# Kernel tuning notes

Hardware: AMD Instinct MI355X
Metric: run time of the kernel (lower is better)

The kernel has to match this reference:

```python
import jax, jax.numpy as jnp
import numpy as np
import math

B, S, IN, H, M = 4, 2048, 256, 128, 128  # mem_dim must equal hidden_size


def _xavier(key, shape):
    fan_in, fan_out = shape[0], shape[-1]
    lim = math.sqrt(6.0 / (fan_in + fan_out))
    return jax.random.uniform(key, shape, jnp.float32, -lim, lim)


def setup_inputs() -> dict:
    key = jax.random.key(0)
    ks = jax.random.split(key, 8)
    return dict(
        x=jax.random.normal(ks[0], (B, S, IN), jnp.float32),
        c0=jnp.zeros((M, M), jnp.float32),   # init_hidden matrix memory
        n0=jnp.zeros((M, 1), jnp.float32),   # init_hidden normalizer
        w_q=_xavier(ks[1], (IN, H)), b_q=jnp.zeros((H,), jnp.float32),
        w_k=_xavier(ks[2], (IN, M)), b_k=jnp.zeros((M,), jnp.float32),
        w_v=_xavier(ks[3], (IN, M)), b_v=jnp.zeros((M,), jnp.float32),
        w_i=_xavier(ks[4], (IN, 1)), b_i=jnp.zeros((1,), jnp.float32),
        w_f=_xavier(ks[5], (IN, 1)), b_f=jnp.zeros((1,), jnp.float32),
        w_o=_xavier(ks[6], (IN, H)), b_o=jnp.zeros((H,), jnp.float32),
    )


def reference(x, c0, n0, w_q, b_q, w_k, b_k, w_v, b_v, w_i, b_i, w_f, b_f, w_o, b_o):
    Bb, Ss, Ii = x.shape
    Mm = w_k.shape[1]
    Hh = w_q.shape[1]
    xf = x.reshape(Bb * Ss, Ii)                                  # [N, IN]
    q = xf @ w_q + b_q                                           # [N, H]
    k = (xf @ w_k + b_k) * (1.0 / math.sqrt(Mm))                 # [N, M]
    v = xf @ w_v + b_v                                           # [N, M]
    i_t = jnp.exp(xf @ w_i + b_i)                                # [N, 1]
    f_t = jax.nn.sigmoid(xf @ w_f + b_f)                         # [N, 1]
    # Original loop never updates c_prev: c_t[n] = f[n]*c0 + i[n]*outer(v[n], k[n])
    c = f_t[:, :, None] * c0[None] + i_t[:, :, None] * (v[:, :, None] * k[:, None, :])  # [N, M, M]
    n = f_t[:, :, None] * n0[None] + i_t[:, :, None] * k[:, :, None]                    # [N, M, 1]
    c = c.reshape(Bb, Ss, Mm, Mm)
    n = n.reshape(Bb, Ss, Mm, 1)
    q4 = q.reshape(Bb, Ss, Hh)
    nq = jnp.einsum('bsm,bsm->bs', n[..., 0], q4)                # n^T q
    denom = jnp.maximum(jnp.abs(nq), 1.0)[..., None]             # max(|n^T q|, 1)
    h_tilde = jnp.einsum('bsmk,bsk->bsm', c, q4) / denom         # (c_t q) / denom
    o = jax.nn.sigmoid(xf @ w_o + b_o).reshape(Bb, Ss, Hh)
    h = o * h_tilde                                              # [B, S, H]
    return (h, c, n)
```

## Files before the change

kernel.cpp:

```cpp
#include <hip/hip_runtime.h>
#include <math.h>

#define B_    4
#define S_    2048
#define IN_   256
#define H_    128
#define M_    128
#define NROWS (B_ * S_)
#define RPB   16
#define GRP   4
#define NGRP  4
#define TPB   512
#define XPAD  260

typedef float f4_t __attribute__((ext_vector_type(4)));

__global__ __launch_bounds__(TPB) void xlstm_pipe(
    const float* __restrict__ x,
    const float* __restrict__ c0,
    const float* __restrict__ n0,
    const float* __restrict__ w_q, const float* __restrict__ b_q,
    const float* __restrict__ w_k, const float* __restrict__ b_k,
    const float* __restrict__ w_v, const float* __restrict__ b_v,
    const float* __restrict__ w_i, const float* __restrict__ b_i,
    const float* __restrict__ w_f, const float* __restrict__ b_f,
    const float* __restrict__ w_o, const float* __restrict__ b_o,
    float* __restrict__ out_h,
    float* __restrict__ out_c,
    float* __restrict__ out_n)
{
    __shared__ float xs[RPB][XPAD];
    __shared__ float bq[2][GRP][M_];
    __shared__ float bk[2][GRP][M_];
    __shared__ float bv[2][GRP][M_];
    __shared__ float bo[2][GRP][M_];
    __shared__ float itf[RPB][2];
    __shared__ float scalb[2][GRP][2];

    const int t    = threadIdx.x;
    const int row0 = blockIdx.x * RPB;
    const bool prod = (t < 256);

    for (int p4 = t; p4 < RPB * IN_ / 4; p4 += TPB) {
        int p = p4 * 4;
        float4 v = *(const float4*)(x + (size_t)row0 * IN_ + p);
        *(float4*)&xs[p >> 8][p & 255] = v;
    }
    __syncthreads();

    const int cg  = t & 31;
    const int mat = (t >> 5) & 3;
    const int rh  = (t >> 7) & 1;
    const int c4  = cg * 4;
    const int col = t & 127;
    const float* W    = (mat==0)? w_q : (mat==1)? w_k : (mat==2)? w_v : w_o;
    const float* BIAS = (mat==0)? b_q : (mat==1)? b_k : (mat==2)? b_v : b_o;
    const f4_t bias4 = *(const f4_t*)(BIAS + c4);
    const float kscale = 0.08838834764831843f;

    const int ct = t & 255;

    float c0qA = 0.f, c0qB = 0.f;

    #pragma unroll 1
    for (int s = 0; s <= NGRP; ++s) {
        if (prod) {
            if (s == 0) {
                const int gr = t >> 4, gseg = t & 15;
                const float* xrow = &xs[gr][gseg * 16];
                float pi = 0.f, pf = 0.f;
                #pragma unroll
                for (int u = 0; u < 4; ++u) {
                    float4 xv  = *(const float4*)(xrow + u * 4);
                    float4 wiv = *(const float4*)(w_i + gseg * 16 + u * 4);
                    float4 wfv = *(const float4*)(w_f + gseg * 16 + u * 4);
                    pi = fmaf(xv.x,wiv.x, fmaf(xv.y,wiv.y, fmaf(xv.z,wiv.z, fmaf(xv.w,wiv.w, pi))));
                    pf = fmaf(xv.x,wfv.x, fmaf(xv.y,wfv.y, fmaf(xv.z,wfv.z, fmaf(xv.w,wfv.w, pf))));
                }
                #pragma unroll
                for (int mm = 1; mm < 16; mm <<= 1) { pi += __shfl_xor(pi, mm); pf += __shfl_xor(pf, mm); }
                if (gseg == 0) {
                    itf[gr][0] = __expf(pi + b_i[0]);
                    itf[gr][1] = 1.f / (1.f + __expf(-(pf + b_f[0])));
                }
            }
            if (s > 0) {
                const int b = (s - 1) & 1;
                #pragma unroll
                for (int rr = 0; rr < 2; ++rr) {
                    const int lrow = rh * 2 + rr;
                    const int row  = (s - 1) * GRP + lrow;
                    const size_t grow = (size_t)(row0 + row);
                    const float iv = itf[row][0], fv = itf[row][1];
                    out_n[grow * M_ + col] = fmaf(fv, n0[col], iv * bk[b][lrow][col]);
                    const float kq  = scalb[b][lrow][0];
                    const float n0q = scalb[b][lrow][1];
                    const float nq = fmaf(fv, n0q, iv * kq);
                    const float denom = fmaxf(fabsf(nq), 1.f);
                    const float c0q = rr ? c0qB : c0qA;
                    const float ht = fmaf(fv, c0q, iv * bv[b][lrow][col] * kq) / denom;
                    out_h[grow * H_ + col] = bo[b][lrow][col] * ht;
                }
            }
            if (s < NGRP) {
                const int b  = s & 1;
                const int r0 = s * GRP + rh * 2;
                f4_t acc0 = (f4_t){0.f,0.f,0.f,0.f};
                f4_t acc1 = (f4_t){0.f,0.f,0.f,0.f};
                #pragma unroll 4
                for (int it = 0; it < 64; ++it) {
                    const int k0 = it * 4;
                    const float* wp = W + (size_t)k0 * H_ + c4;
                    f4_t w0 = *(const f4_t*)(wp);
                    f4_t w1 = *(const f4_t*)(wp + H_);
                    f4_t w2 = *(const f4_t*)(wp + 2 * H_);
                    f4_t w3 = *(const f4_t*)(wp + 3 * H_);
                    f4_t xv0 = *(const f4_t*)&xs[r0][k0];
                    f4_t xv1 = *(const f4_t*)&xs[r0 + 1][k0];
                    acc0 += xv0.x*w0 + xv0.y*w1 + xv0.z*w2 + xv0.w*w3;
                    acc1 += xv1.x*w0 + xv1.y*w1 + xv1.z*w2 + xv1.w*w3;
                }
                acc0 += bias4; acc1 += bias4;
                if (mat == 1) { acc0 *= kscale; acc1 *= kscale; }
                if (mat == 3) {
                    acc0.x = 1.f/(1.f+__expf(-acc0.x)); acc0.y = 1.f/(1.f+__expf(-acc0.y));
                    acc0.z = 1.f/(1.f+__expf(-acc0.z)); acc0.w = 1.f/(1.f+__expf(-acc0.w));
                    acc1.x = 1.f/(1.f+__expf(-acc1.x)); acc1.y = 1.f/(1.f+__expf(-acc1.y));
                    acc1.z = 1.f/(1.f+__expf(-acc1.z)); acc1.w = 1.f/(1.f+__expf(-acc1.w));
                }
                float (*DST)[M_] = (mat==0)? bq[b] : (mat==1)? bk[b] : (mat==2)? bv[b] : bo[b];
                const int lr = rh * 2;
                *(f4_t*)&DST[lr][c4]     = acc0;
                *(f4_t*)&DST[lr + 1][c4] = acc1;
            }
        } else if (s > 0) {
            const int b     = (s - 1) & 1;
            const int gbase = (s - 1) * GRP;
            const int base  = ct * 4;
            const int j     = base & 127;
            #pragma unroll 2
            for (int ch = 0; ch < 16; ++ch) {
                const int p = (ch << 10) + base;
                const int m = p >> 7;
                f4_t c0v = *(const f4_t*)(c0 + p);
                #pragma unroll
                for (int r = 0; r < 2; ++r) {
                    const int row = gbase + r;
                    f4_t k4 = *(const f4_t*)&bk[b][r][j];
                    float sf = itf[row][0] * bv[b][r][m];
                    f4_t o4 = itf[row][1] * c0v + sf * k4;
                    __builtin_nontemporal_store(o4,
                        (f4_t*)(out_c + (size_t)(row0 + row) * (M_ * M_) + p));
                }
            }
        }
        __syncthreads();
        if (prod) {
            if (s < NGRP) {
                const int b  = s & 1;
                const int lr = rh * 2;
                float a0 = 0.f, a1 = 0.f;
                const float* c0row = c0 + (size_t)col * M_;
                #pragma unroll 2
                for (int j4 = 0; j4 < M_; j4 += 4) {
                    f4_t w4 = *(const f4_t*)(c0row + j4);
                    f4_t qa = *(const f4_t*)&bq[b][lr][j4];
                    f4_t qb = *(const f4_t*)&bq[b][lr + 1][j4];
                    a0 = fmaf(w4.x,qa.x, fmaf(w4.y,qa.y, fmaf(w4.z,qa.z, fmaf(w4.w,qa.w, a0))));
                    a1 = fmaf(w4.x,qb.x, fmaf(w4.y,qb.y, fmaf(w4.z,qb.z, fmaf(w4.w,qb.w, a1))));
                }
                c0qA = a0; c0qB = a1;
                const int wv = t >> 6;
                const int l  = t & 63;
                const float ka  = bk[b][wv][l], kb2 = bk[b][wv][l + 64];
                const float qa2 = bq[b][wv][l], qb2 = bq[b][wv][l + 64];
                float pkq = fmaf(ka, qa2, kb2 * qb2);
                float pnq = fmaf(n0[l], qa2, n0[l + 64] * qb2);
                #pragma unroll
                for (int mm = 1; mm < 64; mm <<= 1) { pkq += __shfl_xor(pkq, mm); pnq += __shfl_xor(pnq, mm); }
                if (l == 0) { scalb[b][wv][0] = pkq; scalb[b][wv][1] = pnq; }
            }
        } else if (s > 0) {
            const int b     = (s - 1) & 1;
            const int gbase = (s - 1) * GRP;
            const int base  = ct * 4;
            const int j     = base & 127;
            #pragma unroll 2
            for (int ch = 0; ch < 16; ++ch) {
                const int p = (ch << 10) + base;
                const int m = p >> 7;
                f4_t c0v = *(const f4_t*)(c0 + p);
                #pragma unroll
                for (int r = 2; r < 4; ++r) {
                    const int row = gbase + r;
                    f4_t k4 = *(const f4_t*)&bk[b][r][j];
                    float sf = itf[row][0] * bv[b][r][m];
                    f4_t o4 = itf[row][1] * c0v + sf * k4;
                    __builtin_nontemporal_store(o4,
                        (f4_t*)(out_c + (size_t)(row0 + row) * (M_ * M_) + p));
                }
            }
        }
        __syncthreads();
    }
}

extern "C" void kernel_launch(void* const* d_in, const int* in_sizes, int n_in,
                              void* d_out, int out_size, void* d_ws, size_t ws_size,
                              hipStream_t stream) {
    const float* x   = (const float*)d_in[0];
    const float* c0  = (const float*)d_in[1];
    const float* n0  = (const float*)d_in[2];
    const float* w_q = (const float*)d_in[3];  const float* b_q = (const float*)d_in[4];
    const float* w_k = (const float*)d_in[5];  const float* b_k = (const float*)d_in[6];
    const float* w_v = (const float*)d_in[7];  const float* b_v = (const float*)d_in[8];
    const float* w_i = (const float*)d_in[9];  const float* b_i = (const float*)d_in[10];
    const float* w_f = (const float*)d_in[11]; const float* b_f = (const float*)d_in[12];
    const float* w_o = (const float*)d_in[13]; const float* b_o = (const float*)d_in[14];

    float* out   = (float*)d_out;
    float* out_h = out;
    float* out_c = out + (size_t)NROWS * H_;
    float* out_n = out_c + (size_t)NROWS * M_ * M_;

    hipLaunchKernelGGL(xlstm_pipe, dim3(NROWS / RPB), dim3(TPB), 0, stream,
                       x, c0, n0, w_q, b_q, w_k, b_k, w_v, b_v,
                       w_i, b_i, w_f, b_f, w_o, b_o,
                       out_h, out_c, out_n);
}
```

Before: 138.3 us.

## Merge pipeline stages to one barrier per step and cache c0 in registers

After: 235.5 us. 1.7x slower.

```diff
diff --git a/kernel.cpp b/kernel.cpp
--- a/kernel.cpp
+++ b/kernel.cpp
@@ -35,7 +35,6 @@
     __shared__ float bv[2][GRP][M_];
     __shared__ float bo[2][GRP][M_];
     __shared__ float itf[RPB][2];
-    __shared__ float scalb[2][GRP][2];
 
     const int t    = threadIdx.x;
     const int row0 = blockIdx.x * RPB;
@@ -46,21 +45,26 @@
         float4 v = *(const float4*)(x + (size_t)row0 * IN_ + p);
         *(float4*)&xs[p >> 8][p & 255] = v;
     }
-    __syncthreads();
 
     const int cg  = t & 31;
     const int mat = (t >> 5) & 3;
     const int rh  = (t >> 7) & 1;
     const int c4  = cg * 4;
     const int col = t & 127;
+    const int l   = t & 63;
     const float* W    = (mat==0)? w_q : (mat==1)? w_k : (mat==2)? w_v : w_o;
     const float* BIAS = (mat==0)? b_q : (mat==1)? b_k : (mat==2)? b_v : b_o;
     const f4_t bias4 = *(const f4_t*)(BIAS + c4);
     const float kscale = 0.08838834764831843f;
-
-    const int ct = t & 255;
-
-    float c0qA = 0.f, c0qB = 0.f;
+    const float n0c = n0[col];
+    const float n0l = n0[l];
+    const float n0h = n0[l + 64];
+
+    const int ct   = t & 255;
+    const int base = ct * 4;
+    const int jj   = base & 127;
+
+    __syncthreads();
 
     #pragma unroll 1
     for (int s = 0; s <= NGRP; ++s) {
@@ -82,24 +86,6 @@
                 if (gseg == 0) {
                     itf[gr][0] = __expf(pi + b_i[0]);
                     itf[gr][1] = 1.f / (1.f + __expf(-(pf + b_f[0])));
-                }
-            }
-            if (s > 0) {
-                const int b = (s - 1) & 1;
-                #pragma unroll
-                for (int rr = 0; rr < 2; ++rr) {
-                    const int lrow = rh * 2 + rr;
-                    const int row  = (s - 1) * GRP + lrow;
-                    const size_t grow = (size_t)(row0 + row);
-                    const float iv = itf[row][0], fv = itf[row][1];
-                    out_n[grow * M_ + col] = fmaf(fv, n0[col], iv * bk[b][lrow][col]);
-                    const float kq  = scalb[b][lrow][0];
-                    const float n0q = scalb[b][lrow][1];
-                    const float nq = fmaf(fv, n0q, iv * kq);
-                    const float denom = fmaxf(fabsf(nq), 1.f);
-                    const float c0q = rr ? c0qB : c0qA;
-                    const float ht = fmaf(fv, c0q, iv * bv[b][lrow][col] * kq) / denom;
-                    out_h[grow * H_ + col] = bo[b][lrow][col] * ht;
                 }
             }
             if (s < NGRP) {
@@ -133,31 +119,8 @@
                 *(f4_t*)&DST[lr][c4]     = acc0;
                 *(f4_t*)&DST[lr + 1][c4] = acc1;
             }
-        } else if (s > 0) {
-            const int b     = (s - 1) & 1;
-            const int gbase = (s - 1) * GRP;
-            const int base  = ct * 4;
-            const int j     = base & 127;
-            #pragma unroll 2
-            for (int ch = 0; ch < 16; ++ch) {
-                const int p = (ch << 10) + base;
-                const int m = p >> 7;
-                f4_t c0v = *(const f4_t*)(c0 + p);
-                #pragma unroll
-                for (int r = 0; r < 2; ++r) {
-                    const int row = gbase + r;
-                    f4_t k4 = *(const f4_t*)&bk[b][r][j];
-                    float sf = itf[row][0] * bv[b][r][m];
-                    f4_t o4 = itf[row][1] * c0v + sf * k4;
-                    __builtin_nontemporal_store(o4,
-                        (f4_t*)(out_c + (size_t)(row0 + row) * (M_ * M_) + p));
-                }
-            }
-        }
-        __syncthreads();
-        if (prod) {
-            if (s < NGRP) {
-                const int b  = s & 1;
+            if (s > 0) {
+                const int b  = (s - 1) & 1;
                 const int lr = rh * 2;
                 float a0 = 0.f, a1 = 0.f;
                 const float* c0row = c0 + (size_t)col * M_;
@@ -169,35 +132,65 @@
                     a0 = fmaf(w4.x,qa.x, fmaf(w4.y,qa.y, fmaf(w4.z,qa.z, fmaf(w4.w,qa.w, a0))));
                     a1 = fmaf(w4.x,qb.x, fmaf(w4.y,qb.y, fmaf(w4.z,qb.z, fmaf(w4.w,qb.w, a1))));
                 }
-                c0qA = a0; c0qB = a1;
-                const int wv = t >> 6;
-                const int l  = t & 63;
-                const float ka  = bk[b][wv][l], kb2 = bk[b][wv][l + 64];
-                const float qa2 = bq[b][wv][l], qb2 = bq[b][wv][l + 64];
-                float pkq = fmaf(ka, qa2, kb2 * qb2);
-                float pnq = fmaf(n0[l], qa2, n0[l + 64] * qb2);
-                #pragma unroll
-                for (int mm = 1; mm < 64; mm <<= 1) { pkq += __shfl_xor(pkq, mm); pnq += __shfl_xor(pnq, mm); }
-                if (l == 0) { scalb[b][wv][0] = pkq; scalb[b][wv][1] = pnq; }
+                float pkq0, pnq0, pkq1, pnq1;
+                {
+                    float ka0 = bk[b][lr][l],     kh0 = bk[b][lr][l + 64];
+                    float qa0 = bq[b][lr][l],     qh0 = bq[b][lr][l + 64];
+                    float ka1 = bk[b][lr + 1][l], kh1 = bk[b][lr + 1][l + 64];
+                    float qa1 = bq[b][lr + 1][l], qh1 = bq[b][lr + 1][l + 64];
+                    pkq0 = fmaf(ka0, qa0, kh0 * qh0);
+                    pnq0 = fmaf(n0l, qa0, n0h * qh0);
+                    pkq1 = fmaf(ka1, qa1, kh1 * qh1);
+                    pnq1 = fmaf(n0l, qa1, n0h * qh1);
+                    #pragma unroll
+                    for (int mm = 1; mm < 64; mm <<= 1) {
+                        pkq0 += __shfl_xor(pkq0, mm); pnq0 += __shfl_xor(pnq0, mm);
+                        pkq1 += __shfl_xor(pkq1, mm); pnq1 += __shfl_xor(pnq1, mm);
+                    }
+                }
+                #pragma unroll
+                for (int rr = 0; rr < 2; ++rr) {
+                    const int lrow = lr + rr;
+                    const int row  = (s - 1) * GRP + lrow;
+                    const size_t grow = (size_t)(row0 + row);
+                    const float iv = itf[row][0], fv = itf[row][1];
+                    const float kq  = rr ? pkq1 : pkq0;
+                    const float n0q = rr ? pnq1 : pnq0;
+                    out_n[grow * M_ + col] = fmaf(fv, n0c, iv * bk[b][lrow][col]);
+                    const float nq = fmaf(fv, n0q, iv * kq);
+                    const float denom = fmaxf(fabsf(nq), 1.f);
+                    const float c0q = rr ? a1 : a0;
+                    const float ht = fmaf(fv, c0q, iv * bv[b][lrow][col] * kq) / denom;
+                    out_h[grow * H_ + col] = bo[b][lrow][col] * ht;
+                }
             }
         } else if (s > 0) {
             const int b     = (s - 1) & 1;
             const int gbase = (s - 1) * GRP;
-            const int base  = ct * 4;
-            const int j     = base & 127;
+
+            f4_t c0r[16];
+            #pragma unroll
+            for (int ch = 0; ch < 16; ++ch)
+                c0r[ch] = *(const f4_t*)(c0 + (ch << 10) + base);
+
+            float ifr[GRP], ffr[GRP];
+            #pragma unroll
+            for (int r = 0; r < GRP; ++r) {
+                ifr[r] = itf[gbase + r][0];
+                ffr[r] = itf[gbase + r][1];
+            }
+
             #pragma unroll 2
             for (int ch = 0; ch < 16; ++ch) {
                 const int p = (ch << 10) + base;
                 const int m = p >> 7;
-                f4_t c0v = *(const f4_t*)(c0 + p);
-                #pragma unroll
-                for (int r = 2; r < 4; ++r) {
-                    const int row = gbase + r;
-                    f4_t k4 = *(const f4_t*)&bk[b][r][j];
-                    float sf = itf[row][0] * bv[b][r][m];
-                    f4_t o4 = itf[row][1] * c0v + sf * k4;
+                #pragma unroll
+                for (int r = 0; r < GRP; ++r) {
+                    f4_t k4 = *(const f4_t*)&bk[b][r][jj];
+                    float sf = ifr[r] * bv[b][r][m];
+                    f4_t o4 = ffr[r] * c0r[ch] + sf * k4;
                     __builtin_nontemporal_store(o4,
-                        (f4_t*)(out_c + (size_t)(row0 + row) * (M_ * M_) + p));
+                        (f4_t*)(out_c + (size_t)(row0 + gbase + r) * (M_ * M_) + p));
                 }
             }
         }
```
